# Optimization experiments

Hardware: AMD Instinct MI355X
Metric: run time of the kernel (lower is better)

## Reference

```python
import jax, jax.numpy as jnp
import numpy as np

B, N, T, D = 4, 1000, 12, 64
HID, EF = 128, 64
E = 64000
STEP = 0.1

def setup_inputs() -> dict:
    key = jax.random.key(0)
    ks = jax.random.split(key, 16)
    s = 0.05
    return {
        'x': jax.random.normal(ks[0], (B, N, T, D), dtype=jnp.float32),
        'batch_idx': jax.random.randint(ks[1], (E,), 0, B, dtype=jnp.int32),
        'sender_idx': jax.random.randint(ks[2], (E,), 0, N, dtype=jnp.int32),
        'receiver_idx': jax.random.randint(ks[3], (E,), 0, N, dtype=jnp.int32),
        'A1_w': jax.random.normal(ks[4], (D, HID), dtype=jnp.float32) * s,
        'A1_b': jax.random.normal(ks[5], (HID,), dtype=jnp.float32) * s,
        'A2_w': jax.random.normal(ks[6], (D, HID), dtype=jnp.float32) * s,
        'A2_b': jax.random.normal(ks[7], (HID,), dtype=jnp.float32) * s,
        'A3_w': jax.random.normal(ks[8], (HID, EF), dtype=jnp.float32) * s,
        'A3_b': jax.random.normal(ks[9], (EF,), dtype=jnp.float32) * s,
        'A4_w': jax.random.normal(ks[10], (EF, D), dtype=jnp.float32) * s,
        'A4_b': jax.random.normal(ks[11], (D,), dtype=jnp.float32) * s,
    }

def reference(x, batch_idx, sender_idx, receiver_idx,
              A1_w, A1_b, A2_w, A2_b, A3_w, A3_b, A4_w, A4_b):
    # x: [B, N, T, D]; edge list gathers (equivalent to adj.nonzero)
    x_sender = x[batch_idx, sender_idx]      # [E, T, D]
    x_receiver = x[batch_idx, receiver_idx]  # [E, T, D]

    def edge_mlp(a, b):
        # A3(relu(A1(a) + A2(b))), applied per edge-time element
        h = jax.nn.relu(a @ A1_w + A1_b + b @ A2_w + A2_b)
        return h @ A3_w + A3_b

    z_ij = edge_mlp(x_sender, x_receiver)
    z_ji = edge_mlp(x_receiver, x_sender)
    v_ij_pre = jax.nn.relu(z_ij - z_ji) @ A4_w + A4_b  # [E, T, D]

    seg_send = batch_idx * N + sender_idx  # [E]
    # numerically-stable segment softmax over outgoing edges of each sender
    max_logits = jax.ops.segment_max(v_ij_pre, seg_send, num_segments=B * N)
    exp_centered = jnp.exp(v_ij_pre - max_logits[seg_send])
    denom = jax.ops.segment_sum(exp_centered, seg_send, num_segments=B * N)
    v_ij = exp_centered / (denom[seg_send] + 1e-12)  # [E, T, D]

    messages = v_ij * x_sender
    seg_recv = batch_idx * N + receiver_idx
    inbound = jax.ops.segment_sum(messages, seg_recv, num_segments=B * N)
    inbound = inbound.reshape(B, N, T, D)

    x_updated = x + STEP * (inbound - x)
    return x_updated, v_ij
```

## Files before the change

### kernel.cpp

```cpp
#include <hip/hip_runtime.h>
#include <math.h>

#define BB 4
#define NN 1000
#define TT 12
#define DD 64
#define HIDN 128
#define EFN 64
#define EE 64000
#define BN (BB*NN)
#define ROWS (BN*TT)
#define TD (TT*DD)
#define TD4 (TD/4)
#define STEPF 0.1f
#define MAXSEG 28
#define ELDS 40

typedef _Float16 f16x8 __attribute__((ext_vector_type(8)));
typedef float f32x4 __attribute__((ext_vector_type(4)));

__device__ __forceinline__ unsigned short f2h(float x) {
    _Float16 h = (_Float16)x;
    return __builtin_bit_cast(unsigned short, h);
}
__device__ __forceinline__ float h2f(unsigned short u) {
    return (float)__builtin_bit_cast(_Float16, u);
}

__global__ __launch_bounds__(256) void k_zero(int* __restrict__ p, int n) {
    int i = blockIdx.x * 256 + threadIdx.x;
    if (i < n) p[i] = 0;
}

__global__ __launch_bounds__(256) void k_count(const int* __restrict__ bi,
                                               const int* __restrict__ si,
                                               const int* __restrict__ ri,
                                               int* __restrict__ cnt_s,
                                               int* __restrict__ cnt_r) {
    int e = blockIdx.x * 256 + threadIdx.x;
    if (e < EE) {
        int b = bi[e];
        atomicAdd(&cnt_s[b * NN + si[e]], 1);
        atomicAdd(&cnt_r[b * NN + ri[e]], 1);
    }
}

__global__ __launch_bounds__(256) void k_scan(const int* __restrict__ cnt_s,
                                              const int* __restrict__ cnt_r,
                                              int* __restrict__ rp_s, int* __restrict__ rp_r,
                                              int* __restrict__ cur_s, int* __restrict__ cur_r) {
    const int* cnt = blockIdx.x ? cnt_r : cnt_s;
    int* rp  = blockIdx.x ? rp_r  : rp_s;
    int* cur = blockIdx.x ? cur_r : cur_s;
    __shared__ int part[256];
    int tid = threadIdx.x;
    const int chunk = 16;
    int bgn = tid * chunk;
    int end = min(bgn + chunk, BN);
    int s = 0;
    for (int i = bgn; i < end; ++i) s += cnt[i];
    part[tid] = s;
    __syncthreads();
    for (int off = 1; off < 256; off <<= 1) {
        int v = part[tid];
        if (tid >= off) v += part[tid - off];
        __syncthreads();
        part[tid] = v;
        __syncthreads();
    }
    int run = tid ? part[tid - 1] : 0;
    for (int i = bgn; i < end; ++i) { rp[i] = run; cur[i] = run; run += cnt[i]; }
    if (tid == 255) rp[BN] = part[255];
}

__global__ __launch_bounds__(256) void k_fill(const int* __restrict__ bi,
                                              const int* __restrict__ si,
                                              const int* __restrict__ ri,
                                              int* __restrict__ cur_s, int* __restrict__ cur_r,
                                              int* __restrict__ el_s, int* __restrict__ el_r) {
    int e = blockIdx.x * 256 + threadIdx.x;
    if (e < EE) {
        int b = bi[e];
        int ps = atomicAdd(&cur_s[b * NN + si[e]], 1);
        el_s[ps] = e;
        int pr = atomicAdd(&cur_r[b * NN + ri[e]], 1);
        el_r[pr] = e;
    }
}

__global__ __launch_bounds__(256) void k_prep_w(const float* __restrict__ A3_w,
                                                const float* __restrict__ A4_w,
                                                unsigned short* __restrict__ W3f,
                                                unsigned short* __restrict__ W4f) {
    int i = blockIdx.x * 256 + threadIdx.x;
    if (i < 8192) {
        int j = i & 7, lane = (i >> 3) & 63, nt = (i >> 9) & 3, kt = i >> 11;
        int k = kt * 32 + (lane >> 4) * 8 + j;
        int n = nt * 16 + (lane & 15);
        W3f[i] = f2h(A3_w[k * 64 + n]);
    } else if (i < 12288) {
        int ii = i - 8192;
        int j = ii & 7, lane = (ii >> 3) & 63, nt = (ii >> 9) & 3, kt = ii >> 11;
        int k = kt * 32 + (lane >> 4) * 8 + j;
        int n = nt * 16 + (lane & 15);
        W4f[ii] = f2h(A4_w[k * 64 + n]);
    }
}

__global__ __launch_bounds__(256) void k_node_proj(const float* __restrict__ x,
                                                   const float* __restrict__ A1_w,
                                                   const float* __restrict__ A1_b,
                                                   const float* __restrict__ A2_w,
                                                   const float* __restrict__ A2_b,
                                                   unsigned short* __restrict__ Q1,
                                                   unsigned short* __restrict__ Q2) {
    __shared__ float xs[16][64];
    int tid = threadIdx.x;
    int row0 = blockIdx.x * 16;
    {
        int i = tid * 4;
        int r = i >> 6, k = i & 63;
        *(float4*)&xs[r][k] = *(const float4*)&x[(size_t)(row0 + r) * 64 + k];
    }
    __syncthreads();
    int h = tid & 127;
    int w = tid >> 7;
    const float* W = w ? A2_w : A1_w;
    float bias = w ? A2_b[h] : A1_b[h];
    float acc[16];
#pragma unroll
    for (int r = 0; r < 16; ++r) acc[r] = 0.f;
    for (int k = 0; k < 64; ++k) {
        float wv = W[k * 128 + h];
#pragma unroll
        for (int r = 0; r < 16; ++r) acc[r] += xs[r][k] * wv;
    }
    unsigned short* Qo = w ? Q2 : Q1;
    for (int r = 0; r < 16; ++r) Qo[(size_t)(row0 + r) * 128 + h] = f2h(acc[r] + bias);
}

__global__ __launch_bounds__(256)
void k_edge_seg(const unsigned short* __restrict__ Q1,
                const unsigned short* __restrict__ Q2,
                const int* __restrict__ ri,
                const int* __restrict__ rp_s,
                const int* __restrict__ el_s,
                const unsigned short* __restrict__ W3f,
                const unsigned short* __restrict__ W4f,
                const float* __restrict__ A4_b,
                float* __restrict__ v) {
    __shared__ unsigned short Vseg[MAXSEG][12][64];
    __shared__ __align__(16) _Float16 Hs[4][16][72];
    __shared__ __align__(16) _Float16 W4s[4096];
    __shared__ int e_lds[ELDS];
    __shared__ int rn_lds[ELDS];

    int seg = blockIdx.x;
    int beg = rp_s[seg], end = rp_s[seg + 1];
    int S = end - beg;
    if (S == 0) return;

    int tid  = threadIdx.x;
    int lane = tid & 63;
    int wv   = tid >> 6;
    int quad = lane >> 4;
    int m    = lane & 15;
    int kbase = quad * 8;
    int b    = seg / NN;

    for (int i = tid; i < 512; i += 256)
        *(f16x8*)&W4s[i * 8] = *(const f16x8*)(const void*)&W4f[i * 8];
    if (tid < ELDS && tid < S) {
        int e = el_s[beg + tid];
        e_lds[tid] = e;
        rn_lds[tid] = b * NN + ri[e];
    }

    f16x8 w3[4][4];
#pragma unroll
    for (int kt = 0; kt < 4; ++kt)
#pragma unroll
        for (int nt = 0; nt < 4; ++nt)
            w3[kt][nt] = *(const f16x8*)(const void*)&W3f[((kt * 4 + nt) * 64 + lane) * 8];
    float b4[4];
#pragma unroll
    for (int nt = 0; nt < 4; ++nt) b4[nt] = A4_b[nt * 16 + m];

    const f16x8 hz = {0, 0, 0, 0, 0, 0, 0, 0};

    f16x8 s1[4], s2[4];
    if (m < 12) {
        const unsigned short* p1 = Q1 + (size_t)seg * (TT * HIDN) + m * 128 + kbase;
        const unsigned short* p2 = Q2 + (size_t)seg * (TT * HIDN) + m * 128 + kbase;
#pragma unroll
        for (int kt = 0; kt < 4; ++kt) {
            s1[kt] = *(const f16x8*)(const void*)(p1 + kt * 32);
            s2[kt] = *(const f16x8*)(const void*)(p2 + kt * 32);
        }
    } else {
#pragma unroll
        for (int kt = 0; kt < 4; ++kt) { s1[kt] = hz; s2[kt] = hz; }
    }

    __syncthreads();

    for (int li = wv; li < S; li += 4) {
        int e, rn;
        if (li < ELDS) { e = e_lds[li]; rn = rn_lds[li]; }
        else           { e = el_s[beg + li]; rn = b * NN + ri[e]; }

        const unsigned short* pr1 = Q1 + (size_t)rn * (TT * HIDN) + m * 128 + kbase;
        const unsigned short* pr2 = Q2 + (size_t)rn * (TT * HIDN) + m * 128 + kbase;

        f32x4 acc[4];
#pragma unroll
        for (int nt = 0; nt < 4; ++nt) acc[nt] = (f32x4){0.f, 0.f, 0.f, 0.f};
#pragma unroll
        for (int kt = 0; kt < 4; ++kt) {
            f16x8 g;
            if (m < 12) {
                f16x8 r1 = *(const f16x8*)(const void*)(pr1 + kt * 32);
                f16x8 r2 = *(const f16x8*)(const void*)(pr2 + kt * 32);
                f16x8 a = s1[kt] + r2;
                f16x8 c = r1 + s2[kt];
                g = __builtin_elementwise_max(a, hz)
                  - __builtin_elementwise_max(c, hz);
            } else {
                g = hz;
            }
#pragma unroll
            for (int nt = 0; nt < 4; ++nt)
                acc[nt] = __builtin_amdgcn_mfma_f32_16x16x32_f16(g, w3[kt][nt], acc[nt], 0, 0, 0);
        }

#pragma unroll
        for (int nt = 0; nt < 4; ++nt)
#pragma unroll
            for (int r = 0; r < 4; ++r)
                Hs[wv][quad * 4 + r][nt * 16 + m] = (_Float16)fmaxf(acc[nt][r], 0.f);

        const _Float16* hp = &Hs[wv][m][kbase];
        f16x8 hf0 = *(const f16x8*)hp;
        f16x8 hf1 = *(const f16x8*)(hp + 32);

#pragma unroll
        for (int nt = 0; nt < 4; ++nt) {
            f32x4 o = (f32x4){b4[nt], b4[nt], b4[nt], b4[nt]};
            o = __builtin_amdgcn_mfma_f32_16x16x32_f16(hf0, *(const f16x8*)&W4s[(nt * 64 + lane) * 8], o, 0, 0, 0);
            o = __builtin_amdgcn_mfma_f32_16x16x32_f16(hf1, *(const f16x8*)&W4s[((4 + nt) * 64 + lane) * 8], o, 0, 0, 0);
            if (quad < 3) {
                if (li < MAXSEG) {
                    int cc = ((nt ^ quad) << 4) | m;
#pragma unroll
                    for (int r = 0; r < 4; ++r)
                        Vseg[li][quad * 4 + r][cc] = f2h(o[r]);
                } else {
                    size_t ebase = (size_t)e * TD;
#pragma unroll
                    for (int r = 0; r < 4; ++r)
                        v[ebase + (quad * 4 + r) * 64 + nt * 16 + m] = o[r];
                }
            }
        }
    }
    __syncthreads();

    int d  = tid & 63;
    int tb = tid >> 6;
    int nL = min(S, MAXSEG);
    int dd[3];
#pragma unroll
    for (int jj = 0; jj < 3; ++jj) dd[jj] = d ^ (jj << 4);

    float mj[3] = {-1e30f, -1e30f, -1e30f};
    for (int i = 0; i < nL; ++i) {
#pragma unroll
        for (int jj = 0; jj < 3; ++jj)
            mj[jj] = fmaxf(mj[jj], h2f(Vseg[i][tb + 4 * jj][dd[jj]]));
    }
    for (int i = MAXSEG; i < S; ++i) {
        int e = (i < ELDS) ? e_lds[i] : el_s[beg + i];
        size_t ebase = (size_t)e * TD;
#pragma unroll
        for (int jj = 0; jj < 3; ++jj)
            mj[jj] = fmaxf(mj[jj], v[ebase + (tb + 4 * jj) * 64 + d]);
    }

    float sj[3] = {0.f, 0.f, 0.f};
    for (int i = 0; i < nL; ++i) {
#pragma unroll
        for (int jj = 0; jj < 3; ++jj)
            sj[jj] += __expf(h2f(Vseg[i][tb + 4 * jj][dd[jj]]) - mj[jj]);
    }
    for (int i = MAXSEG; i < S; ++i) {
        int e = (i < ELDS) ? e_lds[i] : el_s[beg + i];
        size_t ebase = (size_t)e * TD;
#pragma unroll
        for (int jj = 0; jj < 3; ++jj)
            sj[jj] += __expf(v[ebase + (tb + 4 * jj) * 64 + d] - mj[jj]);
    }

    float inv[3];
#pragma unroll
    for (int jj = 0; jj < 3; ++jj) inv[jj] = 1.f / (sj[jj] + 1e-12f);

    for (int i = 0; i < nL; ++i) {
        int e = (i < ELDS) ? e_lds[i] : el_s[beg + i];
        size_t ebase = (size_t)e * TD;
#pragma unroll
        for (int jj = 0; jj < 3; ++jj)
            v[ebase + (tb + 4 * jj) * 64 + d] =
                __expf(h2f(Vseg[i][tb + 4 * jj][dd[jj]]) - mj[jj]) * inv[jj];
    }
    for (int i = MAXSEG; i < S; ++i) {
        int e = (i < ELDS) ? e_lds[i] : el_s[beg + i];
        size_t ebase = (size_t)e * TD;
#pragma unroll
        for (int jj = 0; jj < 3; ++jj) {
            size_t a = ebase + (tb + 4 * jj) * 64 + d;
            v[a] = __expf(v[a] - mj[jj]) * inv[jj];
        }
    }
}

__global__ __launch_bounds__(192) void k_aggregate(const int* __restrict__ rp_r,
                                                   const int* __restrict__ el_r,
                                                   const int* __restrict__ si,
                                                   const float* __restrict__ x,
                                                   const float* __restrict__ v,
                                                   float* __restrict__ xout) {
    int node = blockIdx.x;
    int beg = rp_r[node], end = rp_r[node + 1];
    int tid = threadIdx.x;
    int b = node / NN;
    __shared__ int e_l[192];
    __shared__ int sb_l[192];
    const float4* v4 = (const float4*)v;
    const float4* x4 = (const float4*)x;
    float4 acc = {0.f, 0.f, 0.f, 0.f};
    for (int c = beg; c < end; c += 192) {
        int cnt = min(end - c, 192);
        if (tid < cnt) {
            int e = el_r[c + tid];
            e_l[tid] = e;
            sb_l[tid] = (b * NN + si[e]) * TD4;
        }
        __syncthreads();
        for (int i = 0; i < cnt; ++i) {
            float4 vv = v4[(size_t)e_l[i] * TD4 + tid];
            float4 xx = x4[(size_t)sb_l[i] + tid];
            acc.x += vv.x * xx.x;
            acc.y += vv.y * xx.y;
            acc.z += vv.z * xx.z;
            acc.w += vv.w * xx.w;
        }
        __syncthreads();
    }
    size_t nb = (size_t)node * TD4 + tid;
    float4 xv = x4[nb];
    float4 o;
    o.x = xv.x + STEPF * (acc.x - xv.x);
    o.y = xv.y + STEPF * (acc.y - xv.y);
    o.z = xv.z + STEPF * (acc.z - xv.z);
    o.w = xv.w + STEPF * (acc.w - xv.w);
    ((float4*)xout)[nb] = o;
}

extern "C" void kernel_launch(void* const* d_in, const int* in_sizes, int n_in,
                              void* d_out, int out_size, void* d_ws, size_t ws_size,
                              hipStream_t stream) {
    const float* x    = (const float*)d_in[0];
    const int*   bi   = (const int*)d_in[1];
    const int*   si   = (const int*)d_in[2];
    const int*   ri   = (const int*)d_in[3];
    const float* A1_w = (const float*)d_in[4];
    const float* A1_b = (const float*)d_in[5];
    const float* A2_w = (const float*)d_in[6];
    const float* A2_b = (const float*)d_in[7];
    const float* A3_w = (const float*)d_in[8];
    const float* A4_w = (const float*)d_in[10];
    const float* A4_b = (const float*)d_in[11];

    float* xout = (float*)d_out;
    float* v    = (float*)d_out + (size_t)BN * TD;

    unsigned short* Q1  = (unsigned short*)d_ws;
    unsigned short* Q2  = Q1 + (size_t)ROWS * HIDN;
    unsigned short* W3f = Q2 + (size_t)ROWS * HIDN;
    unsigned short* W4f = W3f + 8192;
    int* cnt_s = (int*)(W4f + 4096);
    int* cnt_r = cnt_s + BN;
    int* rp_s  = cnt_r + BN;
    int* rp_r  = rp_s + BN + 1;
    int* cur_s = rp_r + BN + 1;
    int* cur_r = cur_s + BN;
    int* el_s  = cur_r + BN;
    int* el_r  = el_s + EE;

    k_zero<<<(2 * BN + 255) / 256, 256, 0, stream>>>(cnt_s, 2 * BN);
    k_count<<<EE / 256, 256, 0, stream>>>(bi, si, ri, cnt_s, cnt_r);
    k_scan<<<2, 256, 0, stream>>>(cnt_s, cnt_r, rp_s, rp_r, cur_s, cur_r);
    k_fill<<<EE / 256, 256, 0, stream>>>(bi, si, ri, cur_s, cur_r, el_s, el_r);
    k_prep_w<<<48, 256, 0, stream>>>(A3_w, A4_w, W3f, W4f);
    k_node_proj<<<ROWS / 16, 256, 0, stream>>>(x, A1_w, A1_b, A2_w, A2_b, Q1, Q2);
    k_edge_seg<<<BN, 256, 0, stream>>>(Q1, Q2, ri, rp_s, el_s, W3f, W4f, A4_b, v);
    k_aggregate<<<BN, 192, 0, stream>>>(rp_r, el_r, si, x, v, xout);
}
```

Before: 450.5 us.

## Use MFMA for node projection, pair edges in edge kernel, unroll aggregation

Node projection now runs as f16 MFMA on pre-packed A1/A2 weight fragments instead of scalar fp32 FMAs, and x is converted to f16 on the fly. The edge-segment kernel processes two edges per wave per iteration so the gathers and MFMA work of one edge can overlap the other's. The aggregation loop is unrolled by four to put more loads in flight. The costs are higher register pressure in the edge kernel and some extra precision loss from rounding x to f16.

```diff
diff --git a/kernel.cpp b/kernel.cpp
--- a/kernel.cpp
+++ b/kernel.cpp
@@ -90,8 +90,12 @@
 
 __global__ __launch_bounds__(256) void k_prep_w(const float* __restrict__ A3_w,
                                                 const float* __restrict__ A4_w,
+                                                const float* __restrict__ A1_w,
+                                                const float* __restrict__ A2_w,
                                                 unsigned short* __restrict__ W3f,
-                                                unsigned short* __restrict__ W4f) {
+                                                unsigned short* __restrict__ W4f,
+                                                unsigned short* __restrict__ W1f,
+                                                unsigned short* __restrict__ W2f) {
     int i = blockIdx.x * 256 + threadIdx.x;
     if (i < 8192) {
         int j = i & 7, lane = (i >> 3) & 63, nt = (i >> 9) & 3, kt = i >> 11;
@@ -104,39 +108,76 @@
         int k = kt * 32 + (lane >> 4) * 8 + j;
         int n = nt * 16 + (lane & 15);
         W4f[ii] = f2h(A4_w[k * 64 + n]);
+    } else if (i < 20480) {
+        int ii = i - 12288;
+        int j = ii & 7, lane = (ii >> 3) & 63, nt = (ii >> 9) & 7, kt = ii >> 12;
+        int k = kt * 32 + (lane >> 4) * 8 + j;
+        int n = nt * 16 + (lane & 15);
+        W1f[ii] = f2h(A1_w[k * 128 + n]);
+    } else {
+        int ii = i - 20480;
+        int j = ii & 7, lane = (ii >> 3) & 63, nt = (ii >> 9) & 7, kt = ii >> 12;
+        int k = kt * 32 + (lane >> 4) * 8 + j;
+        int n = nt * 16 + (lane & 15);
+        W2f[ii] = f2h(A2_w[k * 128 + n]);
     }
 }
 
 __global__ __launch_bounds__(256) void k_node_proj(const float* __restrict__ x,
-                                                   const float* __restrict__ A1_w,
+                                                   const unsigned short* __restrict__ W1f,
+                                                   const unsigned short* __restrict__ W2f,
                                                    const float* __restrict__ A1_b,
-                                                   const float* __restrict__ A2_w,
                                                    const float* __restrict__ A2_b,
                                                    unsigned short* __restrict__ Q1,
                                                    unsigned short* __restrict__ Q2) {
-    __shared__ float xs[16][64];
-    int tid = threadIdx.x;
-    int row0 = blockIdx.x * 16;
-    {
-        int i = tid * 4;
-        int r = i >> 6, k = i & 63;
-        *(float4*)&xs[r][k] = *(const float4*)&x[(size_t)(row0 + r) * 64 + k];
-    }
-    __syncthreads();
-    int h = tid & 127;
-    int w = tid >> 7;
-    const float* W = w ? A2_w : A1_w;
-    float bias = w ? A2_b[h] : A1_b[h];
-    float acc[16];
-#pragma unroll
-    for (int r = 0; r < 16; ++r) acc[r] = 0.f;
-    for (int k = 0; k < 64; ++k) {
-        float wv = W[k * 128 + h];
-#pragma unroll
-        for (int r = 0; r < 16; ++r) acc[r] += xs[r][k] * wv;
-    }
-    unsigned short* Qo = w ? Q2 : Q1;
-    for (int r = 0; r < 16; ++r) Qo[(size_t)(row0 + r) * 128 + h] = f2h(acc[r] + bias);
+    int tid  = threadIdx.x;
+    int lane = tid & 63;
+    int wvv  = tid >> 6;
+    int mat  = wvv >> 1;
+    int rt   = blockIdx.x * 32 + (wvv & 1) * 16;
+    int quad = lane >> 4;
+    int m    = lane & 15;
+
+    const unsigned short* Wf = mat ? W2f : W1f;
+    const float* bias = mat ? A2_b : A1_b;
+    unsigned short* Qo = mat ? Q2 : Q1;
+
+    f16x8 wf[2][8];
+#pragma unroll
+    for (int kt = 0; kt < 2; ++kt)
+#pragma unroll
+        for (int nt = 0; nt < 8; ++nt)
+            wf[kt][nt] = *(const f16x8*)(const void*)&Wf[((kt * 8 + nt) * 64 + lane) * 8];
+
+    float bb[8];
+#pragma unroll
+    for (int nt = 0; nt < 8; ++nt) bb[nt] = bias[nt * 16 + m];
+
+    const float* xr = x + (size_t)(rt + m) * 64;
+    f16x8 af[2];
+#pragma unroll
+    for (int kt = 0; kt < 2; ++kt) {
+        float4 u0 = *(const float4*)(xr + kt * 32 + quad * 8);
+        float4 u1 = *(const float4*)(xr + kt * 32 + quad * 8 + 4);
+        f16x8 a;
+        a[0] = (_Float16)u0.x; a[1] = (_Float16)u0.y; a[2] = (_Float16)u0.z; a[3] = (_Float16)u0.w;
+        a[4] = (_Float16)u1.x; a[5] = (_Float16)u1.y; a[6] = (_Float16)u1.z; a[7] = (_Float16)u1.w;
+        af[kt] = a;
+    }
+
+    f32x4 acc[8];
+#pragma unroll
+    for (int nt = 0; nt < 8; ++nt) {
+        f32x4 o = (f32x4){0.f, 0.f, 0.f, 0.f};
+        o = __builtin_amdgcn_mfma_f32_16x16x32_f16(af[0], wf[0][nt], o, 0, 0, 0);
+        o = __builtin_amdgcn_mfma_f32_16x16x32_f16(af[1], wf[1][nt], o, 0, 0, 0);
+        acc[nt] = o;
+    }
+#pragma unroll
+    for (int nt = 0; nt < 8; ++nt)
+#pragma unroll
+        for (int r = 0; r < 4; ++r)
+            Qo[(size_t)(rt + quad * 4 + r) * 128 + nt * 16 + m] = f2h(acc[nt][r] + bb[nt]);
 }
 
 __global__ __launch_bounds__(256)
@@ -204,64 +245,114 @@
 
     __syncthreads();
 
-    for (int li = wv; li < S; li += 4) {
-        int e, rn;
-        if (li < ELDS) { e = e_lds[li]; rn = rn_lds[li]; }
-        else           { e = el_s[beg + li]; rn = b * NN + ri[e]; }
-
-        const unsigned short* pr1 = Q1 + (size_t)rn * (TT * HIDN) + m * 128 + kbase;
-        const unsigned short* pr2 = Q2 + (size_t)rn * (TT * HIDN) + m * 128 + kbase;
-
-        f32x4 acc[4];
+    auto build_g = [&](const f16x8* r1, const f16x8* r2, f16x8* g) {
+        if (m < 12) {
+#pragma unroll
+            for (int kt = 0; kt < 4; ++kt) {
+                f16x8 a = s1[kt] + r2[kt];
+                f16x8 c = r1[kt] + s2[kt];
+                g[kt] = __builtin_elementwise_max(a, hz)
+                      - __builtin_elementwise_max(c, hz);
+            }
+        } else {
+#pragma unroll
+            for (int kt = 0; kt < 4; ++kt) g[kt] = hz;
+        }
+    };
+    auto zmfma = [&](const f16x8* g, f32x4* acc) {
 #pragma unroll
         for (int nt = 0; nt < 4; ++nt) acc[nt] = (f32x4){0.f, 0.f, 0.f, 0.f};
 #pragma unroll
-        for (int kt = 0; kt < 4; ++kt) {
-            f16x8 g;
-            if (m < 12) {
-                f16x8 r1 = *(const f16x8*)(const void*)(pr1 + kt * 32);
-                f16x8 r2 = *(const f16x8*)(const void*)(pr2 + kt * 32);
-                f16x8 a = s1[kt] + r2;
-                f16x8 c = r1 + s2[kt];
-                g = __builtin_elementwise_max(a, hz)
-                  - __builtin_elementwise_max(c, hz);
-            } else {
-                g = hz;
-            }
+        for (int kt = 0; kt < 4; ++kt)
 #pragma unroll
             for (int nt = 0; nt < 4; ++nt)
-                acc[nt] = __builtin_amdgcn_mfma_f32_16x16x32_f16(g, w3[kt][nt], acc[nt], 0, 0, 0);
-        }
-
+                acc[nt] = __builtin_amdgcn_mfma_f32_16x16x32_f16(g[kt], w3[kt][nt], acc[nt], 0, 0, 0);
+    };
+    auto h_store = [&](const f32x4* acc) {
 #pragma unroll
         for (int nt = 0; nt < 4; ++nt)
 #pragma unroll
             for (int r = 0; r < 4; ++r)
                 Hs[wv][quad * 4 + r][nt * 16 + m] = (_Float16)fmaxf(acc[nt][r], 0.f);
-
+    };
+    auto finish = [&](int lx, int ex) {
         const _Float16* hp = &Hs[wv][m][kbase];
         f16x8 hf0 = *(const f16x8*)hp;
         f16x8 hf1 = *(const f16x8*)(hp + 32);
-
 #pragma unroll
         for (int nt = 0; nt < 4; ++nt) {
             f32x4 o = (f32x4){b4[nt], b4[nt], b4[nt], b4[nt]};
             o = __builtin_amdgcn_mfma_f32_16x16x32_f16(hf0, *(const f16x8*)&W4s[(nt * 64 + lane) * 8], o, 0, 0, 0);
             o = __builtin_amdgcn_mfma_f32_16x16x32_f16(hf1, *(const f16x8*)&W4s[((4 + nt) * 64 + lane) * 8], o, 0, 0, 0);
             if (quad < 3) {
-                if (li < MAXSEG) {
+                if (lx < MAXSEG) {
                     int cc = ((nt ^ quad) << 4) | m;
 #pragma unroll
                     for (int r = 0; r < 4; ++r)
-                        Vseg[li][quad * 4 + r][cc] = f2h(o[r]);
+                        Vseg[lx][quad * 4 + r][cc] = f2h(o[r]);
                 } else {
-                    size_t ebase = (size_t)e * TD;
+                    size_t ebase = (size_t)ex * TD;
 #pragma unroll
                     for (int r = 0; r < 4; ++r)
                         v[ebase + (quad * 4 + r) * 64 + nt * 16 + m] = o[r];
                 }
             }
         }
+    };
+
+    int li = wv;
+    for (; li + 4 < S; li += 8) {
+        int liB = li + 4;
+        int eA, rnA, eB, rnB;
+        if (li  < ELDS) { eA = e_lds[li];  rnA = rn_lds[li];  }
+        else            { eA = el_s[beg + li];  rnA = b * NN + ri[eA]; }
+        if (liB < ELDS) { eB = e_lds[liB]; rnB = rn_lds[liB]; }
+        else            { eB = el_s[beg + liB]; rnB = b * NN + ri[eB]; }
+
+        f16x8 ra1[4], ra2[4], rb1[4], rb2[4];
+        if (m < 12) {
+            const unsigned short* pa1 = Q1 + (size_t)rnA * (TT * HIDN) + m * 128 + kbase;
+            const unsigned short* pa2 = Q2 + (size_t)rnA * (TT * HIDN) + m * 128 + kbase;
+            const unsigned short* pb1 = Q1 + (size_t)rnB * (TT * HIDN) + m * 128 + kbase;
+            const unsigned short* pb2 = Q2 + (size_t)rnB * (TT * HIDN) + m * 128 + kbase;
+#pragma unroll
+            for (int kt = 0; kt < 4; ++kt) {
+                ra1[kt] = *(const f16x8*)(const void*)(pa1 + kt * 32);
+                ra2[kt] = *(const f16x8*)(const void*)(pa2 + kt * 32);
+                rb1[kt] = *(const f16x8*)(const void*)(pb1 + kt * 32);
+                rb2[kt] = *(const f16x8*)(const void*)(pb2 + kt * 32);
+            }
+        }
+
+        f16x8 gA[4];  build_g(ra1, ra2, gA);
+        f32x4 accA[4]; zmfma(gA, accA);
+        h_store(accA);
+
+        f16x8 gB[4];  build_g(rb1, rb2, gB);
+        f32x4 accB[4]; zmfma(gB, accB);
+
+        finish(li, eA);
+        h_store(accB);
+        finish(liB, eB);
+    }
+    if (li < S) {
+        int e, rn;
+        if (li < ELDS) { e = e_lds[li]; rn = rn_lds[li]; }
+        else           { e = el_s[beg + li]; rn = b * NN + ri[e]; }
+        f16x8 r1[4], r2[4];
+        if (m < 12) {
+            const unsigned short* pr1 = Q1 + (size_t)rn * (TT * HIDN) + m * 128 + kbase;
+            const unsigned short* pr2 = Q2 + (size_t)rn * (TT * HIDN) + m * 128 + kbase;
+#pragma unroll
+            for (int kt = 0; kt < 4; ++kt) {
+                r1[kt] = *(const f16x8*)(const void*)(pr1 + kt * 32);
+                r2[kt] = *(const f16x8*)(const void*)(pr2 + kt * 32);
+            }
+        }
+        f16x8 g[4];  build_g(r1, r2, g);
+        f32x4 acc[4]; zmfma(g, acc);
+        h_store(acc);
+        finish(li, e);
     }
     __syncthreads();
 
@@ -346,13 +437,26 @@
             sb_l[tid] = (b * NN + si[e]) * TD4;
         }
         __syncthreads();
-        for (int i = 0; i < cnt; ++i) {
+        int i = 0;
+        for (; i + 4 <= cnt; i += 4) {
+            float4 v0 = v4[(size_t)e_l[i    ] * TD4 + tid];
+            float4 x0 = x4[(size_t)sb_l[i   ] + tid];
+            float4 v1 = v4[(size_t)e_l[i + 1] * TD4 + tid];
+            float4 x1 = x4[(size_t)sb_l[i + 1] + tid];
+            float4 v2 = v4[(size_t)e_l[i + 2] * TD4 + tid];
+            float4 x2 = x4[(size_t)sb_l[i + 2] + tid];
+            float4 v3 = v4[(size_t)e_l[i + 3] * TD4 + tid];
+            float4 x3 = x4[(size_t)sb_l[i + 3] + tid];
+            acc.x += v0.x * x0.x; acc.y += v0.y * x0.y; acc.z += v0.z * x0.z; acc.w += v0.w * x0.w;
+            acc.x += v1.x * x1.x; acc.y += v1.y * x1.y; acc.z += v1.z * x1.z; acc.w += v1.w * x1.w;
+            acc.x += v2.x * x2.x; acc.y += v2.y * x2.y; acc.z += v2.z * x2.z; acc.w += v2.w * x2.w;
+            acc.x += v3.x * x3.x; acc.y += v3.y * x3.y; acc.z += v3.z * x3.z; acc.w += v3.w * x3.w;
+        }
+        for (; i < cnt; ++i) {
             float4 vv = v4[(size_t)e_l[i] * TD4 + tid];
             float4 xx = x4[(size_t)sb_l[i] + tid];
-            acc.x += vv.x * xx.x;
-            acc.y += vv.y * xx.y;
-            acc.z += vv.z * xx.z;
-            acc.w += vv.w * xx.w;
+            acc.x += vv.x * xx.x; acc.y += vv.y * xx.y;
+            acc.z += vv.z * xx.z; acc.w += vv.w * xx.w;
         }
         __syncthreads();
     }
@@ -388,7 +492,9 @@
     unsigned short* Q2  = Q1 + (size_t)ROWS * HIDN;
     unsigned short* W3f = Q2 + (size_t)ROWS * HIDN;
     unsigned short* W4f = W3f + 8192;
-    int* cnt_s = (int*)(W4f + 4096);
+    unsigned short* W1f = W4f + 4096;
+    unsigned short* W2f = W1f + 8192;
+    int* cnt_s = (int*)(W2f + 8192);
     int* cnt_r = cnt_s + BN;
     int* rp_s  = cnt_r + BN;
     int* rp_r  = rp_s + BN + 1;
@@ -401,8 +507,8 @@
     k_count<<<EE / 256, 256, 0, stream>>>(bi, si, ri, cnt_s, cnt_r);
     k_scan<<<2, 256, 0, stream>>>(cnt_s, cnt_r, rp_s, rp_r, cur_s, cur_r);
     k_fill<<<EE / 256, 256, 0, stream>>>(bi, si, ri, cur_s, cur_r, el_s, el_r);
-    k_prep_w<<<48, 256, 0, stream>>>(A3_w, A4_w, W3f, W4f);
-    k_node_proj<<<ROWS / 16, 256, 0, stream>>>(x, A1_w, A1_b, A2_w, A2_b, Q1, Q2);
+    k_prep_w<<<112, 256, 0, stream>>>(A3_w, A4_w, A1_w, A2_w, W3f, W4f, W1f, W2f);
+    k_node_proj<<<ROWS / 32, 256, 0, stream>>>(x, W1f, W2f, A1_b, A2_b, Q1, Q2);
     k_edge_seg<<<BN, 256, 0, stream>>>(Q1, Q2, ri, rp_s, el_s, W3f, W4f, A4_b, v);
     k_aggregate<<<BN, 192, 0, stream>>>(rp_r, el_r, si, x, v, xout);
 }
```

After: 495.6 us. 10.0% more time.
